# Kernel tuning notes

Hardware: AMD Instinct MI355X
Metric: run time of the kernel (lower is better)

The kernel has to match this reference:

```python
import jax, jax.numpy as jnp
import numpy as np
import math

N_NODES = 100000
N_EDGES = 3200000
NFEAT = 512
NHID = 256
NCLASS = 16
NLAYERS = 8
LAMDA = 0.5
ALPHA = 0.1


def setup_inputs() -> dict:
    key = jax.random.key(0)
    ks = jax.random.split(key, 10)
    x = jax.random.normal(ks[0], (N_NODES, NFEAT), dtype=jnp.float32)
    edge_src = jax.random.randint(ks[1], (N_EDGES,), 0, N_NODES, dtype=jnp.int32)
    edge_dst = jax.random.randint(ks[2], (N_EDGES,), 0, N_NODES, dtype=jnp.int32)
    edge_w = jax.random.uniform(ks[3], (N_EDGES,), dtype=jnp.float32)
    # fcs[0]: Linear(nfeat, nhidden); fcs[1]: Linear(nhidden, nclass)
    s0 = 1.0 / math.sqrt(NFEAT)
    w0 = jax.random.uniform(ks[4], (NFEAT, NHID), minval=-s0, maxval=s0, dtype=jnp.float32)
    b0 = jax.random.uniform(ks[5], (NHID,), minval=-s0, maxval=s0, dtype=jnp.float32)
    # conv weights: uniform(-1/sqrt(out_features), +), out_features = nhidden
    sc = 1.0 / math.sqrt(NHID)
    conv_w = jax.random.uniform(ks[6], (NLAYERS, NHID, NHID), minval=-sc, maxval=sc, dtype=jnp.float32)
    w1 = jax.random.uniform(ks[7], (NHID, NCLASS), minval=-sc, maxval=sc, dtype=jnp.float32)
    b1 = jax.random.uniform(ks[8], (NCLASS,), minval=-sc, maxval=sc, dtype=jnp.float32)
    return {"x": x, "edge_src": edge_src, "edge_dst": edge_dst, "edge_w": edge_w,
            "w0": w0, "b0": b0, "conv_w": conv_w, "w1": w1, "b1": b1}


def _spmm(edge_src, edge_dst, edge_w, h):
    # torch.spmm(adj, h): out[i] = sum_j adj[i,j] * h[j], adj in COO (dst=row, src=col)
    msgs = edge_w[:, None] * h[edge_src]            # [E, H] irregular gather
    return jax.ops.segment_sum(msgs, edge_dst, num_segments=h.shape[0])


def reference(x, edge_src, edge_dst, edge_w, w0, b0, conv_w, w1, b1):
    # eval mode: F.dropout is identity
    h = jax.nn.relu(x @ w0 + b0)                    # [N, NHID]
    h0 = h
    for i in range(NLAYERS):
        theta = math.log(LAMDA / (i + 1) + 1.0)
        hi = _spmm(edge_src, edge_dst, edge_w, h)   # sparse aggregate
        support = (1.0 - ALPHA) * hi + ALPHA * h0   # initial residual (GCNII)
        out = theta * (support @ conv_w[i]) + (1.0 - theta) * support
        h = jax.nn.relu(out + h)                    # layer residual
    return jax.nn.sigmoid(h @ w1 + b1)              # [N, NCLASS]
```

## Files before the change

kernel.cpp:

```cpp
#include <hip/hip_runtime.h>
#include <math.h>

#define N_NODES 100000
#define N_EDGES 3200000
#define NFEAT 512
#define NHID 256
#define NCLASS 16
#define NLAYERS 8

#define SCAN_CHUNK 1024
#define NB ((N_NODES + SCAN_CHUNK - 1) / SCAN_CHUNK)

__global__ void k_hist(const int* __restrict__ dst, int* __restrict__ cnt) {
  int i = blockIdx.x * 256 + threadIdx.x;
  if (i < N_EDGES) atomicAdd(&cnt[dst[i]], 1);
}

__global__ void k_blocksum(const int* __restrict__ cnt, int* __restrict__ bs) {
  __shared__ int red[256];
  int b = blockIdx.x, t = threadIdx.x;
  int s = 0;
  int base = b * SCAN_CHUNK;
  for (int j = 0; j < 4; ++j) {
    int i = base + t + j * 256;
    if (i < N_NODES) s += cnt[i];
  }
  red[t] = s;
  __syncthreads();
  for (int off = 128; off > 0; off >>= 1) {
    if (t < off) red[t] += red[t + off];
    __syncthreads();
  }
  if (t == 0) bs[b] = red[0];
}

__global__ void k_scan_top(int* __restrict__ bs, int* __restrict__ rp) {
  if (threadIdx.x == 0) {
    int run = 0;
    for (int b = 0; b < NB; ++b) { int v = bs[b]; bs[b] = run; run += v; }
    rp[N_NODES] = run;
  }
}

__global__ void k_scan_write(const int* __restrict__ cnt, const int* __restrict__ bs,
                             int* __restrict__ rp) {
  __shared__ int tot[256];
  int b = blockIdx.x, t = threadIdx.x;
  int base = b * SCAN_CHUNK + t * 4;
  int v0 = 0, v1 = 0, v2 = 0, v3 = 0;
  if (base + 0 < N_NODES) v0 = cnt[base + 0];
  if (base + 1 < N_NODES) v1 = cnt[base + 1];
  if (base + 2 < N_NODES) v2 = cnt[base + 2];
  if (base + 3 < N_NODES) v3 = cnt[base + 3];
  int tsum = v0 + v1 + v2 + v3;
  tot[t] = tsum;
  __syncthreads();
  for (int off = 1; off < 256; off <<= 1) {
    int val = 0;
    if (t >= off) val = tot[t - off];
    __syncthreads();
    if (t >= off) tot[t] += val;
    __syncthreads();
  }
  int excl = tot[t] - tsum + bs[b];
  if (base + 0 < N_NODES) rp[base + 0] = excl;
  if (base + 1 < N_NODES) rp[base + 1] = excl + v0;
  if (base + 2 < N_NODES) rp[base + 2] = excl + v0 + v1;
  if (base + 3 < N_NODES) rp[base + 3] = excl + v0 + v1 + v2;
}

__global__ void k_fill(const int* __restrict__ src, const int* __restrict__ dst,
                       const float* __restrict__ w, const int* __restrict__ rp,
                       int* __restrict__ fill, int* __restrict__ col,
                       float* __restrict__ val) {
  int i = blockIdx.x * 256 + threadIdx.x;
  if (i < N_EDGES) {
    int d = dst[i];
    int pos = rp[d] + atomicAdd(&fill[d], 1);
    col[pos] = src[i];
    val[pos] = w[i];
  }
}

__global__ __launch_bounds__(256)
void k_spmm(const int* __restrict__ rp, const int* __restrict__ col,
            const float* __restrict__ val, const float* __restrict__ h,
            const float* __restrict__ h0, float* __restrict__ sup) {
  int wave = threadIdx.x >> 6;
  int lane = threadIdx.x & 63;
  int node = blockIdx.x * 4 + wave;
  if (node >= N_NODES) return;
  int e0 = rp[node], e1 = rp[node + 1];
  float4 acc = make_float4(0.f, 0.f, 0.f, 0.f);
  const float4* __restrict__ hv = (const float4*)h;
  for (int e = e0; e < e1; ++e) {
    int s = col[e];
    float wv = val[e];
    float4 v = hv[(size_t)s * 64 + lane];
    acc.x += wv * v.x; acc.y += wv * v.y; acc.z += wv * v.z; acc.w += wv * v.w;
  }
  float4 z = ((const float4*)h0)[(size_t)node * 64 + lane];
  float4 o;
  o.x = 0.9f * acc.x + 0.1f * z.x;
  o.y = 0.9f * acc.y + 0.1f * z.y;
  o.z = 0.9f * acc.z + 0.1f * z.z;
  o.w = 0.9f * acc.w + 0.1f * z.w;
  ((float4*)sup)[(size_t)node * 64 + lane] = o;
}

template <int MODE>
__global__ __launch_bounds__(256)
void k_gemm(const float* __restrict__ A, const float* __restrict__ W, int K,
            const float* __restrict__ bias, const float* __restrict__ hin,
            float* __restrict__ out1, float* __restrict__ out2, float theta) {
  __shared__ float As[16][128];
  __shared__ float Bs[16][128];
  int bm = blockIdx.x * 128, bn = blockIdx.y * 128;
  int tid = threadIdx.x;
  int tx = tid & 15, ty = tid >> 4;
  float acc[8][8];
#pragma unroll
  for (int i = 0; i < 8; ++i)
#pragma unroll
    for (int j = 0; j < 8; ++j) acc[i][j] = 0.f;

  for (int kc = 0; kc < K; kc += 16) {
#pragma unroll
    for (int it = 0; it < 2; ++it) {
      int idx = tid + it * 256;
      int m = idx >> 2, q = (idx & 3) * 4;
      int gm = bm + m;
      float4 f = make_float4(0.f, 0.f, 0.f, 0.f);
      if (gm < N_NODES) f = *(const float4*)&A[(size_t)gm * K + kc + q];
      As[q + 0][m] = f.x; As[q + 1][m] = f.y; As[q + 2][m] = f.z; As[q + 3][m] = f.w;
    }
#pragma unroll
    for (int it = 0; it < 2; ++it) {
      int idx = tid + it * 256;
      int kk = idx >> 5, nq = (idx & 31) * 4;
      *(float4*)&Bs[kk][nq] = *(const float4*)&W[(size_t)(kc + kk) * NHID + bn + nq];
    }
    __syncthreads();
#pragma unroll
    for (int k = 0; k < 16; ++k) {
      float a[8], b[8];
      *(float4*)&a[0] = *(const float4*)&As[k][ty * 8];
      *(float4*)&a[4] = *(const float4*)&As[k][ty * 8 + 4];
      *(float4*)&b[0] = *(const float4*)&Bs[k][tx * 8];
      *(float4*)&b[4] = *(const float4*)&Bs[k][tx * 8 + 4];
#pragma unroll
      for (int i = 0; i < 8; ++i)
#pragma unroll
        for (int j = 0; j < 8; ++j) acc[i][j] += a[i] * b[j];
    }
    __syncthreads();
  }

#pragma unroll
  for (int i = 0; i < 8; ++i) {
    int gm = bm + ty * 8 + i;
    if (gm >= N_NODES) continue;
    size_t rowo = (size_t)gm * NHID + bn + tx * 8;
    if (MODE == 0) {
#pragma unroll
      for (int j = 0; j < 8; ++j) {
        float v = acc[i][j] + bias[bn + tx * 8 + j];
        v = fmaxf(v, 0.f);
        out1[rowo + j] = v;
        out2[rowo + j] = v;
      }
    } else {
      float omt = 1.f - theta;
#pragma unroll
      for (int j = 0; j < 8; ++j) {
        float s = A[rowo + j];
        float hv = hin[rowo + j];
        float v = theta * acc[i][j] + omt * s + hv;
        out1[rowo + j] = fmaxf(v, 0.f);
      }
    }
  }
}

__global__ __launch_bounds__(256)
void k_final(const float* __restrict__ h, const float* __restrict__ w1,
             const float* __restrict__ b1, float* __restrict__ out) {
  __shared__ float ws[NHID * NCLASS];
  int t = threadIdx.x;
  for (int i = t; i < NHID * NCLASS; i += 256) ws[i] = w1[i];
  __syncthreads();
  int node = blockIdx.x * 16 + (t >> 4);
  int c = t & 15;
  if (node >= N_NODES) return;
  float acc = b1[c];
  const float* hr = &h[(size_t)node * NHID];
  for (int k = 0; k < NHID; k += 4) {
    float4 hv = *(const float4*)&hr[k];
    acc += hv.x * ws[(k + 0) * NCLASS + c];
    acc += hv.y * ws[(k + 1) * NCLASS + c];
    acc += hv.z * ws[(k + 2) * NCLASS + c];
    acc += hv.w * ws[(k + 3) * NCLASS + c];
  }
  out[(size_t)node * NCLASS + c] = 1.f / (1.f + __expf(-acc));
}

extern "C" void kernel_launch(void* const* d_in, const int* in_sizes, int n_in,
                              void* d_out, int out_size, void* d_ws, size_t ws_size,
                              hipStream_t stream) {
  const float* x        = (const float*)d_in[0];
  const int*   edge_src = (const int*)d_in[1];
  const int*   edge_dst = (const int*)d_in[2];
  const float* edge_w   = (const float*)d_in[3];
  const float* w0       = (const float*)d_in[4];
  const float* b0       = (const float*)d_in[5];
  const float* conv_w   = (const float*)d_in[6];
  const float* w1       = (const float*)d_in[7];
  const float* b1       = (const float*)d_in[8];
  float* out = (float*)d_out;

  char* ws = (char*)d_ws;
  size_t off = 0;
  auto alloc = [&](size_t bytes) {
    size_t o = off;
    off = (off + bytes + 255) & ~(size_t)255;
    return (void*)(ws + o);
  };
  float* h   = (float*)alloc((size_t)N_NODES * NHID * 4);
  float* h0  = (float*)alloc((size_t)N_NODES * NHID * 4);
  float* sup = (float*)alloc((size_t)N_NODES * NHID * 4);
  int*   rp  = (int*)alloc((size_t)(N_NODES + 1) * 4);
  int*   cnt = (int*)alloc((size_t)N_NODES * 4);
  int*   col = (int*)alloc((size_t)N_EDGES * 4);
  float* val = (float*)alloc((size_t)N_EDGES * 4);
  int*   bs  = (int*)alloc((size_t)NB * 4);
  (void)ws_size;

  hipMemsetAsync(cnt, 0, (size_t)N_NODES * 4, stream);
  k_hist<<<(N_EDGES + 255) / 256, 256, 0, stream>>>(edge_dst, cnt);
  k_blocksum<<<NB, 256, 0, stream>>>(cnt, bs);
  k_scan_top<<<1, 64, 0, stream>>>(bs, rp);
  k_scan_write<<<NB, 256, 0, stream>>>(cnt, bs, rp);
  hipMemsetAsync(cnt, 0, (size_t)N_NODES * 4, stream);
  k_fill<<<(N_EDGES + 255) / 256, 256, 0, stream>>>(edge_src, edge_dst, edge_w, rp,
                                                    cnt, col, val);

  dim3 g0((N_NODES + 127) / 128, NHID / 128);
  k_gemm<0><<<g0, 256, 0, stream>>>(x, w0, NFEAT, b0, nullptr, h, h0, 0.f);

  for (int i = 0; i < NLAYERS; ++i) {
    float theta = logf(0.5f / (float)(i + 1) + 1.0f);
    k_spmm<<<(N_NODES + 3) / 4, 256, 0, stream>>>(rp, col, val, h, h0, sup);
    const float* cw = conv_w + (size_t)i * NHID * NHID;
    k_gemm<1><<<g0, 256, 0, stream>>>(sup, cw, NHID, nullptr, h, h, nullptr, theta);
  }

  k_final<<<(N_NODES + 15) / 16, 256, 0, stream>>>(h, w1, b1, out);
}
```

Baseline: 6.126 ms.

## Split SpMM into two feature-half passes with 4-way unrolled edge loop

Each layer's sparse aggregation now runs as two launches, each covering 128 of the 256 hidden features with float2 loads per lane. The gathered working set per pass is halved (about 51 MB instead of 102 MB of h), which is meant to raise cache hit rates on the random neighbour gathers. The edge loop is also unrolled by four with separate accumulators to keep more loads in flight. The cost is reading the CSR col/val arrays twice, an extra launch per layer, and narrower 8-byte per-lane accesses.

```diff
diff --git a/kernel.cpp b/kernel.cpp
--- a/kernel.cpp
+++ b/kernel.cpp
@@ -83,29 +83,51 @@
 }
 
 __global__ __launch_bounds__(256)
-void k_spmm(const int* __restrict__ rp, const int* __restrict__ col,
-            const float* __restrict__ val, const float* __restrict__ h,
-            const float* __restrict__ h0, float* __restrict__ sup) {
+void k_spmm_half(const int* __restrict__ rp, const int* __restrict__ col,
+                 const float* __restrict__ val, const float* __restrict__ h,
+                 const float* __restrict__ h0, float* __restrict__ sup, int f0) {
   int wave = threadIdx.x >> 6;
   int lane = threadIdx.x & 63;
   int node = blockIdx.x * 4 + wave;
   if (node >= N_NODES) return;
   int e0 = rp[node], e1 = rp[node + 1];
-  float4 acc = make_float4(0.f, 0.f, 0.f, 0.f);
-  const float4* __restrict__ hv = (const float4*)h;
-  for (int e = e0; e < e1; ++e) {
-    int s = col[e];
-    float wv = val[e];
-    float4 v = hv[(size_t)s * 64 + lane];
-    acc.x += wv * v.x; acc.y += wv * v.y; acc.z += wv * v.z; acc.w += wv * v.w;
-  }
-  float4 z = ((const float4*)h0)[(size_t)node * 64 + lane];
-  float4 o;
+  const float2* __restrict__ hv = (const float2*)h;
+  int fo = (f0 >> 1) + lane;
+
+  float2 a0 = make_float2(0.f, 0.f);
+  float2 a1 = make_float2(0.f, 0.f);
+  float2 a2 = make_float2(0.f, 0.f);
+  float2 a3 = make_float2(0.f, 0.f);
+
+  int e = e0;
+  for (; e + 4 <= e1; e += 4) {
+    int s0 = col[e], s1 = col[e + 1], s2 = col[e + 2], s3 = col[e + 3];
+    float w0 = val[e], w1 = val[e + 1], w2 = val[e + 2], w3 = val[e + 3];
+    float2 v0 = hv[(size_t)s0 * 128 + fo];
+    float2 v1 = hv[(size_t)s1 * 128 + fo];
+    float2 v2 = hv[(size_t)s2 * 128 + fo];
+    float2 v3 = hv[(size_t)s3 * 128 + fo];
+    a0.x += w0 * v0.x; a0.y += w0 * v0.y;
+    a1.x += w1 * v1.x; a1.y += w1 * v1.y;
+    a2.x += w2 * v2.x; a2.y += w2 * v2.y;
+    a3.x += w3 * v3.x; a3.y += w3 * v3.y;
+  }
+  for (; e < e1; ++e) {
+    int s0 = col[e];
+    float w0 = val[e];
+    float2 v0 = hv[(size_t)s0 * 128 + fo];
+    a0.x += w0 * v0.x; a0.y += w0 * v0.y;
+  }
+
+  float2 acc;
+  acc.x = (a0.x + a1.x) + (a2.x + a3.x);
+  acc.y = (a0.y + a1.y) + (a2.y + a3.y);
+
+  float2 z = ((const float2*)h0)[(size_t)node * 128 + fo];
+  float2 o;
   o.x = 0.9f * acc.x + 0.1f * z.x;
   o.y = 0.9f * acc.y + 0.1f * z.y;
-  o.z = 0.9f * acc.z + 0.1f * z.z;
-  o.w = 0.9f * acc.w + 0.1f * z.w;
-  ((float4*)sup)[(size_t)node * 64 + lane] = o;
+  ((float2*)sup)[(size_t)node * 128 + fo] = o;
 }
 
 template <int MODE>
@@ -249,7 +271,8 @@
 
   for (int i = 0; i < NLAYERS; ++i) {
     float theta = logf(0.5f / (float)(i + 1) + 1.0f);
-    k_spmm<<<(N_NODES + 3) / 4, 256, 0, stream>>>(rp, col, val, h, h0, sup);
+    k_spmm_half<<<(N_NODES + 3) / 4, 256, 0, stream>>>(rp, col, val, h, h0, sup, 0);
+    k_spmm_half<<<(N_NODES + 3) / 4, 256, 0, stream>>>(rp, col, val, h, h0, sup, 128);
     const float* cw = conv_w + (size_t)i * NHID * NHID;
     k_gemm<1><<<g0, 256, 0, stream>>>(sup, cw, NHID, nullptr, h, h, nullptr, theta);
   }
```

Result: no change. 6.098 ms (-0.5%).

## Fuse SpMM aggregation with per-layer GEMM and epilogue into one kernel

Applied to the files above, without the earlier changes.

Each layer now runs one kernel. A block of 128 threads aggregates 32 nodes' neighbour features into a transposed shared-memory tile, then multiplies that tile by the layer weight and applies the residual and ReLU before writing to a ping-pong h buffer. This removes the global write and re-read of the support matrix and one launch per layer. The gather loop is unrolled by 8 with two accumulators to get more loads in flight, and h0 and output use nontemporal accesses. In exchange, the weight matrix is reloaded from memory by every 32-node block, the block is small, and shared-memory use is large, which can lower occupancy. The first GEMM's epilogue is also changed to use vectorised stores.

```diff
diff --git a/kernel.cpp b/kernel.cpp
--- a/kernel.cpp
+++ b/kernel.cpp
@@ -7,9 +7,12 @@
 #define NHID 256
 #define NCLASS 16
 #define NLAYERS 8
+#define TM 32
 
 #define SCAN_CHUNK 1024
 #define NB ((N_NODES + SCAN_CHUNK - 1) / SCAN_CHUNK)
+
+typedef float vf4 __attribute__((ext_vector_type(4)));
 
 __global__ void k_hist(const int* __restrict__ dst, int* __restrict__ cnt) {
   int i = blockIdx.x * 256 + threadIdx.x;
@@ -56,10 +59,10 @@
   tot[t] = tsum;
   __syncthreads();
   for (int off = 1; off < 256; off <<= 1) {
-    int val = 0;
-    if (t >= off) val = tot[t - off];
-    __syncthreads();
-    if (t >= off) tot[t] += val;
+    int v = 0;
+    if (t >= off) v = tot[t - off];
+    __syncthreads();
+    if (t >= off) tot[t] += v;
     __syncthreads();
   }
   int excl = tot[t] - tsum + bs[b];
@@ -82,37 +85,119 @@
   }
 }
 
+__global__ __launch_bounds__(128)
+void k_layer(const int* __restrict__ rp, const int* __restrict__ col,
+             const float* __restrict__ val, const float* __restrict__ h,
+             const float* __restrict__ h0, const float* __restrict__ W,
+             float* __restrict__ out, float theta) {
+  __shared__ float supT[256][36];
+  __shared__ float Bs[16][256];
+  int tid = threadIdx.x;
+  int node0 = blockIdx.x * TM;
+
+  {
+    int wv = tid >> 6, lane = tid & 63;
+    const float4* __restrict__ h4 = (const float4*)h;
+    for (int i = 0; i < 16; ++i) {
+      int nl = wv * 16 + i;
+      int n = node0 + nl;
+      int e0 = rp[n], e1 = rp[n + 1];
+      float4 a0 = make_float4(0.f, 0.f, 0.f, 0.f);
+      float4 a1 = make_float4(0.f, 0.f, 0.f, 0.f);
+      int e = e0;
+      for (; e + 8 <= e1; e += 8) {
+        int   s0 = col[e],     s1 = col[e + 1], s2 = col[e + 2], s3 = col[e + 3];
+        int   s4 = col[e + 4], s5 = col[e + 5], s6 = col[e + 6], s7 = col[e + 7];
+        float w0 = val[e],     w1 = val[e + 1], w2 = val[e + 2], w3 = val[e + 3];
+        float w4 = val[e + 4], w5 = val[e + 5], w6 = val[e + 6], w7 = val[e + 7];
+        float4 v0 = h4[(size_t)s0 * 64 + lane];
+        float4 v1 = h4[(size_t)s1 * 64 + lane];
+        float4 v2 = h4[(size_t)s2 * 64 + lane];
+        float4 v3 = h4[(size_t)s3 * 64 + lane];
+        float4 v4 = h4[(size_t)s4 * 64 + lane];
+        float4 v5 = h4[(size_t)s5 * 64 + lane];
+        float4 v6 = h4[(size_t)s6 * 64 + lane];
+        float4 v7 = h4[(size_t)s7 * 64 + lane];
+        a0.x += w0 * v0.x; a0.y += w0 * v0.y; a0.z += w0 * v0.z; a0.w += w0 * v0.w;
+        a1.x += w1 * v1.x; a1.y += w1 * v1.y; a1.z += w1 * v1.z; a1.w += w1 * v1.w;
+        a0.x += w2 * v2.x; a0.y += w2 * v2.y; a0.z += w2 * v2.z; a0.w += w2 * v2.w;
+        a1.x += w3 * v3.x; a1.y += w3 * v3.y; a1.z += w3 * v3.z; a1.w += w3 * v3.w;
+        a0.x += w4 * v4.x; a0.y += w4 * v4.y; a0.z += w4 * v4.z; a0.w += w4 * v4.w;
+        a1.x += w5 * v5.x; a1.y += w5 * v5.y; a1.z += w5 * v5.z; a1.w += w5 * v5.w;
+        a0.x += w6 * v6.x; a0.y += w6 * v6.y; a0.z += w6 * v6.z; a0.w += w6 * v6.w;
+        a1.x += w7 * v7.x; a1.y += w7 * v7.y; a1.z += w7 * v7.z; a1.w += w7 * v7.w;
+      }
+      for (; e < e1; ++e) {
+        int s0 = col[e];
+        float w0 = val[e];
+        float4 v0 = h4[(size_t)s0 * 64 + lane];
+        a0.x += w0 * v0.x; a0.y += w0 * v0.y; a0.z += w0 * v0.z; a0.w += w0 * v0.w;
+      }
+      vf4 z = __builtin_nontemporal_load((const vf4*)h0 + (size_t)n * 64 + lane);
+      supT[4 * lane + 0][nl] = 0.9f * (a0.x + a1.x) + 0.1f * z.x;
+      supT[4 * lane + 1][nl] = 0.9f * (a0.y + a1.y) + 0.1f * z.y;
+      supT[4 * lane + 2][nl] = 0.9f * (a0.z + a1.z) + 0.1f * z.z;
+      supT[4 * lane + 3][nl] = 0.9f * (a0.w + a1.w) + 0.1f * z.w;
+    }
+  }
+  __syncthreads();
+
+  int tx = tid & 15;
+  int ty = tid >> 4;
+  float acc[4][16];
+#pragma unroll
+  for (int i = 0; i < 4; ++i)
+#pragma unroll
+    for (int j = 0; j < 16; ++j) acc[i][j] = 0.f;
+
+  for (int kc = 0; kc < NHID; kc += 16) {
+    const float4* __restrict__ Wv = (const float4*)(W + (size_t)kc * 256);
+    float4* Bv = (float4*)&Bs[0][0];
+#pragma unroll
+    for (int j = 0; j < 8; ++j) Bv[tid + j * 128] = Wv[tid + j * 128];
+    __syncthreads();
+#pragma unroll
+    for (int k = 0; k < 16; ++k) {
+      float a_[4], b_[16];
+      *(float4*)&a_[0]  = *(const float4*)&supT[kc + k][ty * 4];
+      *(float4*)&b_[0]  = *(const float4*)&Bs[k][tx * 4];
+      *(float4*)&b_[4]  = *(const float4*)&Bs[k][tx * 4 + 64];
+      *(float4*)&b_[8]  = *(const float4*)&Bs[k][tx * 4 + 128];
+      *(float4*)&b_[12] = *(const float4*)&Bs[k][tx * 4 + 192];
+#pragma unroll
+      for (int i = 0; i < 4; ++i)
+#pragma unroll
+        for (int j = 0; j < 16; ++j) acc[i][j] += a_[i] * b_[j];
+    }
+    __syncthreads();
+  }
+
+  float omt = 1.f - theta;
+#pragma unroll
+  for (int i = 0; i < 4; ++i) {
+    int r = ty * 4 + i;
+    int gm = node0 + r;
+    const float* __restrict__ hrow = &h[(size_t)gm * 256];
+#pragma unroll
+    for (int q = 0; q < 4; ++q) {
+      int c = tx * 4 + 64 * q;
+      float4 hv = *(const float4*)&hrow[c];
+      float s0 = supT[c + 0][r], s1 = supT[c + 1][r];
+      float s2 = supT[c + 2][r], s3 = supT[c + 3][r];
+      vf4 o;
+      o.x = fmaxf(theta * acc[i][4 * q + 0] + omt * s0 + hv.x, 0.f);
+      o.y = fmaxf(theta * acc[i][4 * q + 1] + omt * s1 + hv.y, 0.f);
+      o.z = fmaxf(theta * acc[i][4 * q + 2] + omt * s2 + hv.z, 0.f);
+      o.w = fmaxf(theta * acc[i][4 * q + 3] + omt * s3 + hv.w, 0.f);
+      __builtin_nontemporal_store(o, (vf4*)&out[(size_t)gm * 256 + c]);
+    }
+  }
+}
+
 __global__ __launch_bounds__(256)
-void k_spmm(const int* __restrict__ rp, const int* __restrict__ col,
-            const float* __restrict__ val, const float* __restrict__ h,
-            const float* __restrict__ h0, float* __restrict__ sup) {
-  int wave = threadIdx.x >> 6;
-  int lane = threadIdx.x & 63;
-  int node = blockIdx.x * 4 + wave;
-  if (node >= N_NODES) return;
-  int e0 = rp[node], e1 = rp[node + 1];
-  float4 acc = make_float4(0.f, 0.f, 0.f, 0.f);
-  const float4* __restrict__ hv = (const float4*)h;
-  for (int e = e0; e < e1; ++e) {
-    int s = col[e];
-    float wv = val[e];
-    float4 v = hv[(size_t)s * 64 + lane];
-    acc.x += wv * v.x; acc.y += wv * v.y; acc.z += wv * v.z; acc.w += wv * v.w;
-  }
-  float4 z = ((const float4*)h0)[(size_t)node * 64 + lane];
-  float4 o;
-  o.x = 0.9f * acc.x + 0.1f * z.x;
-  o.y = 0.9f * acc.y + 0.1f * z.y;
-  o.z = 0.9f * acc.z + 0.1f * z.z;
-  o.w = 0.9f * acc.w + 0.1f * z.w;
-  ((float4*)sup)[(size_t)node * 64 + lane] = o;
-}
-
-template <int MODE>
-__global__ __launch_bounds__(256)
-void k_gemm(const float* __restrict__ A, const float* __restrict__ W, int K,
-            const float* __restrict__ bias, const float* __restrict__ hin,
-            float* __restrict__ out1, float* __restrict__ out2, float theta) {
+void k_gemm0(const float* __restrict__ A, const float* __restrict__ W,
+             const float* __restrict__ bias, float* __restrict__ out1,
+             float* __restrict__ out2) {
   __shared__ float As[16][128];
   __shared__ float Bs[16][128];
   int bm = blockIdx.x * 128, bn = blockIdx.y * 128;
@@ -124,14 +209,14 @@
 #pragma unroll
     for (int j = 0; j < 8; ++j) acc[i][j] = 0.f;
 
-  for (int kc = 0; kc < K; kc += 16) {
+  for (int kc = 0; kc < NFEAT; kc += 16) {
 #pragma unroll
     for (int it = 0; it < 2; ++it) {
       int idx = tid + it * 256;
       int m = idx >> 2, q = (idx & 3) * 4;
       int gm = bm + m;
       float4 f = make_float4(0.f, 0.f, 0.f, 0.f);
-      if (gm < N_NODES) f = *(const float4*)&A[(size_t)gm * K + kc + q];
+      if (gm < N_NODES) f = *(const float4*)&A[(size_t)gm * NFEAT + kc + q];
       As[q + 0][m] = f.x; As[q + 1][m] = f.y; As[q + 2][m] = f.z; As[q + 3][m] = f.w;
     }
 #pragma unroll
@@ -146,8 +231,8 @@
       float a[8], b[8];
       *(float4*)&a[0] = *(const float4*)&As[k][ty * 8];
       *(float4*)&a[4] = *(const float4*)&As[k][ty * 8 + 4];
-      *(float4*)&b[0] = *(const float4*)&Bs[k][tx * 8];
-      *(float4*)&b[4] = *(const float4*)&Bs[k][tx * 8 + 4];
+      *(float4*)&b[0] = *(const float4*)&Bs[k][tx * 4];
+      *(float4*)&b[4] = *(const float4*)&Bs[k][tx * 4 + 64];
 #pragma unroll
       for (int i = 0; i < 8; ++i)
 #pragma unroll
@@ -156,29 +241,24 @@
     __syncthreads();
   }
 
+  int c0 = bn + tx * 4, c1 = bn + 64 + tx * 4;
 #pragma unroll
   for (int i = 0; i < 8; ++i) {
     int gm = bm + ty * 8 + i;
     if (gm >= N_NODES) continue;
-    size_t rowo = (size_t)gm * NHID + bn + tx * 8;
-    if (MODE == 0) {
-#pragma unroll
-      for (int j = 0; j < 8; ++j) {
-        float v = acc[i][j] + bias[bn + tx * 8 + j];
-        v = fmaxf(v, 0.f);
-        out1[rowo + j] = v;
-        out2[rowo + j] = v;
-      }
-    } else {
-      float omt = 1.f - theta;
-#pragma unroll
-      for (int j = 0; j < 8; ++j) {
-        float s = A[rowo + j];
-        float hv = hin[rowo + j];
-        float v = theta * acc[i][j] + omt * s + hv;
-        out1[rowo + j] = fmaxf(v, 0.f);
-      }
-    }
+    float4 o0, o1;
+    o0.x = fmaxf(acc[i][0] + bias[c0 + 0], 0.f);
+    o0.y = fmaxf(acc[i][1] + bias[c0 + 1], 0.f);
+    o0.z = fmaxf(acc[i][2] + bias[c0 + 2], 0.f);
+    o0.w = fmaxf(acc[i][3] + bias[c0 + 3], 0.f);
+    o1.x = fmaxf(acc[i][4] + bias[c1 + 0], 0.f);
+    o1.y = fmaxf(acc[i][5] + bias[c1 + 1], 0.f);
+    o1.z = fmaxf(acc[i][6] + bias[c1 + 2], 0.f);
+    o1.w = fmaxf(acc[i][7] + bias[c1 + 3], 0.f);
+    *(float4*)&out1[(size_t)gm * NHID + c0] = o0;
+    *(float4*)&out1[(size_t)gm * NHID + c1] = o1;
+    *(float4*)&out2[(size_t)gm * NHID + c0] = o0;
+    *(float4*)&out2[(size_t)gm * NHID + c1] = o1;
   }
 }
 
@@ -225,9 +305,9 @@
     off = (off + bytes + 255) & ~(size_t)255;
     return (void*)(ws + o);
   };
-  float* h   = (float*)alloc((size_t)N_NODES * NHID * 4);
+  float* hA  = (float*)alloc((size_t)N_NODES * NHID * 4);
+  float* hB  = (float*)alloc((size_t)N_NODES * NHID * 4);
   float* h0  = (float*)alloc((size_t)N_NODES * NHID * 4);
-  float* sup = (float*)alloc((size_t)N_NODES * NHID * 4);
   int*   rp  = (int*)alloc((size_t)(N_NODES + 1) * 4);
   int*   cnt = (int*)alloc((size_t)N_NODES * 4);
   int*   col = (int*)alloc((size_t)N_EDGES * 4);
@@ -245,14 +325,15 @@
                                                     cnt, col, val);
 
   dim3 g0((N_NODES + 127) / 128, NHID / 128);
-  k_gemm<0><<<g0, 256, 0, stream>>>(x, w0, NFEAT, b0, nullptr, h, h0, 0.f);
+  k_gemm0<<<g0, 256, 0, stream>>>(x, w0, b0, hA, h0);
 
   for (int i = 0; i < NLAYERS; ++i) {
     float theta = logf(0.5f / (float)(i + 1) + 1.0f);
-    k_spmm<<<(N_NODES + 3) / 4, 256, 0, stream>>>(rp, col, val, h, h0, sup);
+    const float* hin  = (i & 1) ? hB : hA;
+    float*       hout = (i & 1) ? hA : hB;
     const float* cw = conv_w + (size_t)i * NHID * NHID;
-    k_gemm<1><<<g0, 256, 0, stream>>>(sup, cw, NHID, nullptr, h, h, nullptr, theta);
-  }
-
-  k_final<<<(N_NODES + 15) / 16, 256, 0, stream>>>(h, w1, b1, out);
-}
+    k_layer<<<N_NODES / TM, 128, 0, stream>>>(rp, col, val, hin, h0, cw, hout, theta);
+  }
+
+  k_final<<<(N_NODES + 15) / 16, 256, 0, stream>>>(hA, w1, b1, out);
+}
```

After: 7.445 ms. 1.22x slower.
